# Kernel tuning notes

Measured on AMD Instinct MI355X. Metric: run time of the kernel, lower is better.

## Reference

```python
import jax, jax.numpy as jnp
import numpy as np

LOOKUP_WINDOW = 101
OUTPUT_DIM = 128
NUM_BINS = 512


def setup_inputs() -> dict:
    key = jax.random.key(0)
    k1, k2 = jax.random.split(key)
    frames = jax.random.randint(k1, (16, 100, 27, 48, 3), 0, 256, dtype=jnp.int32)
    fc_w = jax.random.normal(k2, (LOOKUP_WINDOW, OUTPUT_DIM), dtype=jnp.float32) * 0.05
    fc_b = jnp.zeros((OUTPUT_DIM,), dtype=jnp.float32)
    return {"frames": frames, "fc_w": fc_w, "fc_b": fc_b}


def _color_histograms(frames):
    # frames: [B, T, H, W, 3] int32 in [0, 256)
    B, T, H, W, C = frames.shape
    f = frames.reshape(B * T, H * W, 3)
    R, G, Bc = f[:, :, 0], f[:, :, 1], f[:, :, 2]
    # 3 bits per channel -> 512 bins
    bins = ((R >> 5) << 6) + ((G >> 5) << 3) + (Bc >> 5)  # [BT, HW]
    frame_prefix = (jnp.arange(B * T, dtype=jnp.int32) << 9)[:, None]
    ids = (bins + frame_prefix).reshape(-1)
    hist = jax.ops.segment_sum(
        jnp.ones_like(ids, dtype=jnp.int32), ids,
        num_segments=B * T * NUM_BINS)
    hist = hist.reshape(B, T, NUM_BINS).astype(jnp.float32)
    # L2-normalize each frame's histogram
    hist = hist / jnp.linalg.norm(hist, axis=2, keepdims=True)
    return hist


def reference(frames, fc_w, fc_b):
    B, T = frames.shape[0], frames.shape[1]
    x = _color_histograms(frames)                  # [B, T, 512]
    sim = jnp.einsum('btd,bsd->bts', x, x)         # [B, T, T]
    half = (LOOKUP_WINDOW - 1) // 2
    padded = jnp.pad(sim, ((0, 0), (0, 0), (half, half)))  # [B, T, T+lw-1]
    # banded gather: band[b, t, w] = padded[b, t, t + w]
    idx = jnp.arange(T)[:, None] + jnp.arange(LOOKUP_WINDOW)[None, :]  # [T, lw]
    band = jnp.take_along_axis(
        padded, jnp.broadcast_to(idx[None], (B, T, LOOKUP_WINDOW)), axis=2)
    # Dense + relu
    return jax.nn.relu(band @ fc_w + fc_b)         # [B, T, 128]
```

## Files before the change

### kernel.cpp

```cpp
#include <hip/hip_runtime.h>
#include <hip/hip_bf16.h>
#include <math.h>

#define B_DIM 16
#define T_DIM 100
#define HW_PIX (27 * 48)
#define NBINS 512
#define WIN 101
#define HALF 50
#define ODIM 128

__global__ __launch_bounds__(256) void hist_kernel(
    const int* __restrict__ frames, float* __restrict__ hist) {
  __shared__ int h[NBINS];
  __shared__ float red[16];

  const int f = blockIdx.x;
  const int tid = threadIdx.x;

  for (int i = tid; i < NBINS; i += 256) h[i] = 0;
  __syncthreads();

  const int* fp = frames + (size_t)f * (HW_PIX * 3);
  for (int p = tid; p < HW_PIX; p += 256) {
    int r = fp[p * 3 + 0];
    int g = fp[p * 3 + 1];
    int b = fp[p * 3 + 2];
    int bin = ((r >> 5) << 6) + ((g >> 5) << 3) + (b >> 5);
    atomicAdd(&h[bin], 1);
  }
  __syncthreads();

  float ss = 0.f;
  for (int i = tid; i < NBINS; i += 256) {
    float v = (float)h[i];
    ss += v * v;
  }
  const int lane = tid & 63, wave = tid >> 6;
#pragma unroll
  for (int off = 32; off > 0; off >>= 1) ss += __shfl_down(ss, off);
  if (lane == 0) red[wave] = ss;
  __syncthreads();
  if (tid == 0) {
    float tot = red[0] + red[1] + red[2] + red[3];
    red[8] = 1.0f / sqrtf(tot);
  }
  __syncthreads();
  const float rn = red[8];

  float* hp = hist + (size_t)f * NBINS;
  for (int i = tid; i < NBINS; i += 256) hp[i] = (float)h[i] * rn;
}

__global__ __launch_bounds__(256) void band_fc_kernel(
    const float* __restrict__ hist, const float* __restrict__ fc_w,
    const float* __restrict__ fc_b, float* __restrict__ out) {
  __shared__ float xq[NBINS];
  __shared__ float band[WIN];

  const int bt = blockIdx.x;
  const int b = bt / T_DIM;
  const int t = bt - b * T_DIM;
  const int tid = threadIdx.x;
  const int lane = tid & 63, wave = tid >> 6;

  const float* xrow = hist + (size_t)bt * NBINS;
  for (int i = tid; i < NBINS; i += 256) xq[i] = xrow[i];
  __syncthreads();

  for (int j = wave; j < WIN; j += 4) {
    const int s = t + j - HALF;
    float dot = 0.f;
    if (s >= 0 && s < T_DIM) {
      const float* xs = hist + ((size_t)(b * T_DIM + s)) * NBINS;
#pragma unroll
      for (int k = 0; k < 8; ++k) {
        dot += xq[lane + 64 * k] * xs[lane + 64 * k];
      }
#pragma unroll
      for (int off = 32; off > 0; off >>= 1) dot += __shfl_down(dot, off);
    }
    if (lane == 0) band[j] = dot;
  }
  __syncthreads();

  if (tid < ODIM) {
    float acc = fc_b[tid];
#pragma unroll 4
    for (int j = 0; j < WIN; ++j) acc += band[j] * fc_w[j * ODIM + tid];
    out[(size_t)bt * ODIM + tid] = fmaxf(acc, 0.f);
  }
}

extern "C" void kernel_launch(void* const* d_in, const int* in_sizes, int n_in,
                              void* d_out, int out_size, void* d_ws, size_t ws_size,
                              hipStream_t stream) {
  const int* frames = (const int*)d_in[0];
  const float* fc_w = (const float*)d_in[1];
  const float* fc_b = (const float*)d_in[2];
  float* out = (float*)d_out;
  float* hist = (float*)d_ws;

  hist_kernel<<<B_DIM * T_DIM, 256, 0, stream>>>(frames, hist);
  band_fc_kernel<<<B_DIM * T_DIM, 256, 0, stream>>>(hist, fc_w, fc_b, out);
}
```

Before: 101.5 us.

## Compute similarity via bf16 MFMA and tile band-FC over 16 timesteps per block

Histograms are written as bf16 into a padded per-batch matrix, and a new kernel computes the full T×T similarity with 16x16x32 bf16 MFMA instructions. The band+FC stage now processes 16 timesteps per block, staging fc_w in LDS and using float4 accumulators. The histogram loop also switches to vectorized int4 loads. This removes the redundant per-timestep dot products and the repeated fc_w reads, at the cost of an extra kernel launch, a global sim buffer and reduced precision from bf16 histograms.

```diff
diff --git a/kernel.cpp b/kernel.cpp
--- a/kernel.cpp
+++ b/kernel.cpp
@@ -4,30 +4,50 @@
 
 #define B_DIM 16
 #define T_DIM 100
+#define TPAD 112
 #define HW_PIX (27 * 48)
 #define NBINS 512
 #define WIN 101
 #define HALF 50
 #define ODIM 128
+#define NTILE 7
+#define BSTRIDE 104
+
+typedef __attribute__((ext_vector_type(8))) short s16x8;
+typedef __attribute__((ext_vector_type(4))) float f32x4;
 
 __global__ __launch_bounds__(256) void hist_kernel(
-    const int* __restrict__ frames, float* __restrict__ hist) {
+    const int* __restrict__ frames, __hip_bfloat16* __restrict__ X16) {
+  const int bid = blockIdx.x;
+  const int tid = threadIdx.x;
+
+  if (bid >= B_DIM * T_DIM) {
+    const int pid = bid - B_DIM * T_DIM;
+    const int b = pid / (TPAD - T_DIM);
+    const int r = pid - b * (TPAD - T_DIM);
+    unsigned int* row = (unsigned int*)(X16 + ((size_t)(b * TPAD + T_DIM + r)) * NBINS);
+    row[tid] = 0u;
+    return;
+  }
+
   __shared__ int h[NBINS];
   __shared__ float red[16];
-
-  const int f = blockIdx.x;
-  const int tid = threadIdx.x;
 
   for (int i = tid; i < NBINS; i += 256) h[i] = 0;
   __syncthreads();
 
-  const int* fp = frames + (size_t)f * (HW_PIX * 3);
-  for (int p = tid; p < HW_PIX; p += 256) {
-    int r = fp[p * 3 + 0];
-    int g = fp[p * 3 + 1];
-    int b = fp[p * 3 + 2];
-    int bin = ((r >> 5) << 6) + ((g >> 5) << 3) + (b >> 5);
-    atomicAdd(&h[bin], 1);
+  const int* fp = frames + (size_t)bid * (HW_PIX * 3);
+  for (int i = tid; i < HW_PIX / 4; i += 256) {
+    const int4* q = (const int4*)(fp + 12 * i);
+    int4 a = q[0], c = q[1], e = q[2];
+    int b0 = ((a.x >> 5) << 6) + ((a.y >> 5) << 3) + (a.z >> 5);
+    int b1 = ((a.w >> 5) << 6) + ((c.x >> 5) << 3) + (c.y >> 5);
+    int b2 = ((c.z >> 5) << 6) + ((c.w >> 5) << 3) + (e.x >> 5);
+    int b3 = ((e.y >> 5) << 6) + ((e.z >> 5) << 3) + (e.w >> 5);
+    atomicAdd(&h[b0], 1);
+    atomicAdd(&h[b1], 1);
+    atomicAdd(&h[b2], 1);
+    atomicAdd(&h[b3], 1);
   }
   __syncthreads();
 
@@ -41,55 +61,101 @@
   for (int off = 32; off > 0; off >>= 1) ss += __shfl_down(ss, off);
   if (lane == 0) red[wave] = ss;
   __syncthreads();
-  if (tid == 0) {
-    float tot = red[0] + red[1] + red[2] + red[3];
-    red[8] = 1.0f / sqrtf(tot);
-  }
+  if (tid == 0) red[8] = 1.0f / sqrtf(red[0] + red[1] + red[2] + red[3]);
   __syncthreads();
   const float rn = red[8];
 
-  float* hp = hist + (size_t)f * NBINS;
-  for (int i = tid; i < NBINS; i += 256) hp[i] = (float)h[i] * rn;
+  const int b = bid / T_DIM;
+  const int t = bid - b * T_DIM;
+  __hip_bfloat16* row = X16 + ((size_t)(b * TPAD + t)) * NBINS;
+  for (int i = tid; i < NBINS; i += 256) row[i] = __float2bfloat16((float)h[i] * rn);
+}
+
+__global__ __launch_bounds__(64) void sim_kernel(
+    const __hip_bfloat16* __restrict__ X16, float* __restrict__ sim) {
+  const int bid = blockIdx.x;
+  const int b = bid / (NTILE * NTILE);
+  const int tile = bid - b * (NTILE * NTILE);
+  const int tm = tile / NTILE, tn = tile - tm * NTILE;
+  const int lane = threadIdx.x;
+  const int m16 = lane & 15, quad = lane >> 4;
+
+  const short* A = (const short*)(X16 + ((size_t)(b * TPAD + tm * 16 + m16)) * NBINS) + quad * 8;
+  const short* Bp = (const short*)(X16 + ((size_t)(b * TPAD + tn * 16 + m16)) * NBINS) + quad * 8;
+
+  f32x4 acc = {0.f, 0.f, 0.f, 0.f};
+#pragma unroll 4
+  for (int k = 0; k < NBINS; k += 32) {
+    s16x8 af = *(const s16x8*)(A + k);
+    s16x8 bf = *(const s16x8*)(Bp + k);
+    acc = __builtin_amdgcn_mfma_f32_16x16x32_bf16(af, bf, acc, 0, 0, 0);
+  }
+
+  const int n = tn * 16 + m16;
+  if (n < T_DIM) {
+    float* srow = sim + (size_t)b * T_DIM * T_DIM + n;
+#pragma unroll
+    for (int r = 0; r < 4; ++r) {
+      int m = tm * 16 + quad * 4 + r;
+      if (m < T_DIM) srow[(size_t)m * T_DIM] = acc[r];
+    }
+  }
 }
 
 __global__ __launch_bounds__(256) void band_fc_kernel(
-    const float* __restrict__ hist, const float* __restrict__ fc_w,
+    const float* __restrict__ sim, const float* __restrict__ fc_w,
     const float* __restrict__ fc_b, float* __restrict__ out) {
-  __shared__ float xq[NBINS];
-  __shared__ float band[WIN];
+  __shared__ __align__(16) float wlds[WIN * ODIM];
+  __shared__ float blds[16 * BSTRIDE];
 
-  const int bt = blockIdx.x;
-  const int b = bt / T_DIM;
-  const int t = bt - b * T_DIM;
+  const int cid = blockIdx.x;
+  const int b = cid / NTILE;
+  const int t0 = (cid - b * NTILE) * 16;
   const int tid = threadIdx.x;
-  const int lane = tid & 63, wave = tid >> 6;
 
-  const float* xrow = hist + (size_t)bt * NBINS;
-  for (int i = tid; i < NBINS; i += 256) xq[i] = xrow[i];
-  __syncthreads();
-
-  for (int j = wave; j < WIN; j += 4) {
-    const int s = t + j - HALF;
-    float dot = 0.f;
-    if (s >= 0 && s < T_DIM) {
-      const float* xs = hist + ((size_t)(b * T_DIM + s)) * NBINS;
-#pragma unroll
-      for (int k = 0; k < 8; ++k) {
-        dot += xq[lane + 64 * k] * xs[lane + 64 * k];
-      }
-#pragma unroll
-      for (int off = 32; off > 0; off >>= 1) dot += __shfl_down(dot, off);
-    }
-    if (lane == 0) band[j] = dot;
+  {
+    const f32x4* src = (const f32x4*)fc_w;
+    f32x4* dst = (f32x4*)wlds;
+    for (int i = tid; i < (WIN * ODIM) / 4; i += 256) dst[i] = src[i];
+  }
+  for (int idx = tid; idx < 16 * WIN; idx += 256) {
+    int tl = idx / WIN;
+    int j = idx - tl * WIN;
+    int t = t0 + tl;
+    int s = t - HALF + j;
+    float v = 0.f;
+    if (t < T_DIM && s >= 0 && s < T_DIM)
+      v = sim[((size_t)b * T_DIM + t) * T_DIM + s];
+    blds[tl * BSTRIDE + j] = v;
   }
   __syncthreads();
 
-  if (tid < ODIM) {
-    float acc = fc_b[tid];
+  const int g4 = tid & 31;
+  const int tl0 = tid >> 5;
+  const int tl1 = tl0 + 8;
+
+  f32x4 acc0 = ((const f32x4*)fc_b)[g4];
+  f32x4 acc1 = acc0;
 #pragma unroll 4
-    for (int j = 0; j < WIN; ++j) acc += band[j] * fc_w[j * ODIM + tid];
-    out[(size_t)bt * ODIM + tid] = fmaxf(acc, 0.f);
+  for (int j = 0; j < WIN; ++j) {
+    f32x4 wv = *(const f32x4*)&wlds[j * ODIM + g4 * 4];
+    float b0 = blds[tl0 * BSTRIDE + j];
+    float b1 = blds[tl1 * BSTRIDE + j];
+    acc0 += wv * b0;
+    acc1 += wv * b1;
   }
+
+#pragma unroll
+  for (int c = 0; c < 4; ++c) {
+    acc0[c] = fmaxf(acc0[c], 0.f);
+    acc1[c] = fmaxf(acc1[c], 0.f);
+  }
+
+  const int t0a = t0 + tl0, t0b = t0 + tl1;
+  if (t0a < T_DIM)
+    *(f32x4*)&out[(((size_t)b * T_DIM + t0a)) * ODIM + g4 * 4] = acc0;
+  if (t0b < T_DIM)
+    *(f32x4*)&out[(((size_t)b * T_DIM + t0b)) * ODIM + g4 * 4] = acc1;
 }
 
 extern "C" void kernel_launch(void* const* d_in, const int* in_sizes, int n_in,
@@ -99,8 +165,11 @@
   const float* fc_w = (const float*)d_in[1];
   const float* fc_b = (const float*)d_in[2];
   float* out = (float*)d_out;
-  float* hist = (float*)d_ws;
 
-  hist_kernel<<<B_DIM * T_DIM, 256, 0, stream>>>(frames, hist);
-  band_fc_kernel<<<B_DIM * T_DIM, 256, 0, stream>>>(hist, fc_w, fc_b, out);
+  __hip_bfloat16* X16 = (__hip_bfloat16*)d_ws;
+  float* sim = (float*)((char*)d_ws + (size_t)B_DIM * TPAD * NBINS * 2);
+
+  hist_kernel<<<B_DIM * T_DIM + B_DIM * (TPAD - T_DIM), 256, 0, stream>>>(frames, X16);
+  sim_kernel<<<B_DIM * NTILE * NTILE, 64, 0, stream>>>(X16, sim);
+  band_fc_kernel<<<B_DIM * NTILE, 256, 0, stream>>>(sim, fc_w, fc_b, out);
 }
```

Measured after the change: 88.32 us. -13.0%, faster.
